# Optimization experiments

Hardware: AMD Instinct MI355X
Metric: run time of the kernel (lower is better)

The kernel has to match this reference:

```python
import jax, jax.numpy as jnp
import numpy as np

B, N, D = 4, 4096, 256

def setup_inputs() -> dict:
    key = jax.random.key(0)
    ks = jax.random.split(key, 7)
    def xavier(k, shape):
        fan_in, fan_out = shape[1], shape[0]
        a = jnp.sqrt(6.0 / (fan_in + fan_out))
        return jax.random.uniform(k, shape, jnp.float32, -a, a)
    return {
        "x": jax.random.normal(ks[0], (B, N, D), jnp.float32),
        "Wq": xavier(ks[1], (D, D)),
        "bq": jnp.zeros((D,), jnp.float32),
        "Wk": xavier(ks[2], (D, D)),
        "bk": jnp.zeros((D,), jnp.float32),
        "Wv": xavier(ks[3], (D, D)),
        "bv": jnp.zeros((D,), jnp.float32),
        "scale": jnp.asarray([jnp.sqrt(jnp.float32(D))]),
    }

def reference(x, Wq, bq, Wk, bk, Wv, bv, scale):
    # nn.Linear: y = x @ W.T + b
    q = jnp.einsum('bnd,ed->bne', x, Wq) + bq
    k = jnp.einsum('bnd,ed->bne', x, Wk) + bk
    v = jnp.einsum('bnd,ed->bne', x, Wv) + bv
    scores = jnp.einsum('bqd,bkd->bqk', q, k) / scale[0]  # [B,N,N]
    attn = jax.nn.softmax(scores, axis=-1)
    out = jnp.einsum('bqk,bkd->bqd', attn, v)
    return out
```

## Files before the change

### kernel.cpp

```cpp
#include <hip/hip_runtime.h>
#include <hip/hip_bf16.h>

typedef unsigned int u32;
typedef unsigned short u16;
typedef __attribute__((ext_vector_type(8))) __bf16 bf8v;
typedef __attribute__((ext_vector_type(16))) float f32x16;
typedef __attribute__((ext_vector_type(8))) u16 u16x8;

__device__ inline u16 f2bf(float f) {
    u32 u = __float_as_uint(f);
    u = (u + 0x7FFF + ((u >> 16) & 1)) >> 16;
    return (u16)u;
}
__device__ inline u32 pk2(float a, float b) {
    return (u32)f2bf(a) | ((u32)f2bf(b) << 16);
}
__device__ inline float bf2f(u16 h) { return __uint_as_float(((u32)h) << 16); }

__device__ inline void dma16(const u16* g, u16* l) {
    __builtin_amdgcn_global_load_lds(
        (const __attribute__((address_space(1))) void*)g,
        (__attribute__((address_space(3))) void*)l, 16, 0, 0);
}

__global__ void cvt_x(const float* __restrict__ src, u16* __restrict__ dst) {
    int g = blockIdx.x * 256 + threadIdx.x;
    int row = g >> 5, cp = g & 31;
    const float* s = src + row * 256 + cp * 8;
    float4 a = *(const float4*)s;
    float4 b = *(const float4*)(s + 4);
    uint4 o;
    o.x = pk2(a.x, a.y); o.y = pk2(a.z, a.w);
    o.z = pk2(b.x, b.y); o.w = pk2(b.z, b.w);
    *(uint4*)(dst + (row >> 5) * 8192 + cp * 256 + (row & 31) * 8) = o;
}

__global__ void cvt_w(const float* __restrict__ wq, const float* __restrict__ wk,
                      const float* __restrict__ wv, u16* __restrict__ dst) {
    const int m = blockIdx.x >> 5;
    const float* src = m == 0 ? wq : m == 1 ? wk : wv;
    int i = ((blockIdx.x & 31) * 256 + threadIdx.x) * 8;
    float4 a = *(const float4*)(src + i);
    float4 b = *(const float4*)(src + i + 4);
    uint4 o;
    o.x = pk2(a.x, a.y); o.y = pk2(a.z, a.w);
    o.z = pk2(b.x, b.y); o.w = pk2(b.z, b.w);
    *(uint4*)(dst + m * 65536 + i) = o;
}

__global__ __launch_bounds__(256) void qkv_proj(
    const u16* __restrict__ xp, const u16* __restrict__ wall,
    const float* __restrict__ bq, const float* __restrict__ bk, const float* __restrict__ bv,
    u16* __restrict__ qp, u16* __restrict__ kp, u16* __restrict__ vp)
{
    const int blk = blockIdx.x;
    const int xcd = blk & 7;
    const int s2 = blk >> 3;
    const int rt = s2 / 12;
    const int yz = s2 % 12;
    const int sel = yz >> 2;
    const int colbase = (yz & 3) * 64;
    const int rowbase0 = (xcd * 16 + rt) * 128;

    const u16* w = wall + sel * 65536;
    const float* bias = sel == 0 ? bq : sel == 1 ? bk : bv;
    const int tid = threadIdx.x;
    const int wave = tid >> 6, lane = tid & 63;
    const int l31 = lane & 31, l5 = lane >> 5;
    const int tg = (rowbase0 >> 5) + wave;

    f32x16 acc0, acc1;
#pragma unroll
    for (int j = 0; j < 16; j++) { acc0[j] = 0.f; acc1[j] = 0.f; }

    const u16* ap  = xp + tg * 8192 + l5 * 256 + l31 * 8;
    const u16* bp0 = w + (colbase + l31) * 256 + l5 * 8;
    const u16* bp1 = bp0 + 32 * 256;
#pragma unroll
    for (int kk = 0; kk < 16; kk++) {
        bf8v af = *(const bf8v*)(ap + kk * 512);
        bf8v b0 = *(const bf8v*)(bp0 + kk * 16);
        bf8v b1 = *(const bf8v*)(bp1 + kk * 16);
        acc0 = __builtin_amdgcn_mfma_f32_32x32x16_bf16(af, b0, acc0, 0, 0, 0);
        acc1 = __builtin_amdgcn_mfma_f32_32x32x16_bf16(af, b1, acc1, 0, 0, 0);
    }

    const float bias0 = bias[colbase + l31], bias1 = bias[colbase + 32 + l31];
    if (sel < 2) {
        u16* base = (sel == 0 ? qp : kp) + tg * 8192;
        const int c0 = (colbase >> 3) + (l31 >> 3), j0 = l31 & 7;
#pragma unroll
        for (int r = 0; r < 16; r++) {
            const int R = (r & 3) + 8 * (r >> 2) + 4 * l5;
            base[c0 * 256 + R * 8 + j0]       = f2bf(acc0[r] + bias0);
            base[(c0 + 4) * 256 + R * 8 + j0] = f2bf(acc1[r] + bias1);
        }
    } else {
        u16* base = vp + tg * 8192;
        const int d0 = colbase + l31, d1 = d0 + 32;
#pragma unroll
        for (int r = 0; r < 16; r++) {
            const int R = (r & 3) + 8 * (r >> 2) + 4 * l5;
            base[(R >> 3) * 2048 + d0 * 8 + (R & 7)] = f2bf(acc0[r] + bias0);
            base[(R >> 3) * 2048 + d1 * 8 + (R & 7)] = f2bf(acc1[r] + bias1);
        }
    }
}

__global__ __launch_bounds__(256, 2) void flash_attn(
    const u16* __restrict__ qp_, const u16* __restrict__ kp_, const u16* __restrict__ vp_,
    const float* __restrict__ scale,
    u16* __restrict__ Opb, float* __restrict__ ml)
{
    __shared__ u16 Ks[2 * 8192];
    __shared__ u16 Vs[2 * 8192];
    __shared__ u16 Ps[4 * 1152];

    const int tid = threadIdx.x;
    const int wave = tid >> 6, lane = tid & 63;
    const int l31 = lane & 31, l5 = lane >> 5;

    const int blk = blockIdx.x;
    const int slot = blk >> 3;
    const int g = (blk & 7) * 2 + (slot >> 5);
    const int qtile = slot & 31;
    const int b = g >> 2, s = g & 3;
    const int qbase = qtile * 128 + wave * 32;
    const float inv_scale = 1.0f / scale[0];

    union { u16x8 u; bf8v v; } oneu;
#pragma unroll
    for (int j = 0; j < 8; j++) oneu.u[j] = 0x3F80;
    const bf8v ones = oneu.v;

    bf8v qf[16];
    {
        const u16* qp = qp_ + (b * 128 + qtile * 4 + wave) * 8192 + l31 * 8;
#pragma unroll
        for (int kk = 0; kk < 16; kk++)
            qf[kk] = *(const bf8v*)(qp + (kk * 2 + l5) * 256);
    }

    f32x16 o[8];
#pragma unroll
    for (int i = 0; i < 8; i++)
#pragma unroll
        for (int j = 0; j < 16; j++) o[i][j] = 0.f;
    f32x16 ls;
#pragma unroll
    for (int j = 0; j < 16; j++) ls[j] = 0.f;

    const u16* kbase = kp_ + (b * 128 + s * 32) * 8192;
    const u16* vbase = vp_ + (b * 128 + s * 32) * 8192;
    u16* pw = Ps + wave * 1152;

#pragma unroll
    for (int j = 0; j < 4; j++) {
        const int i = wave * 4 + j;
        dma16(kbase + i * 512 + lane * 8, Ks + i * 512);
    }
#pragma unroll
    for (int j = 0; j < 4; j++) {
        const int i = wave * 4 + j;
        dma16(vbase + i * 512 + lane * 8, Vs + i * 512);
    }
#pragma unroll
    for (int j = 0; j < 4; j++) {
        const int i = wave * 4 + j;
        dma16(kbase + 8192 + i * 512 + lane * 8, Ks + 8192 + i * 512);
    }
    asm volatile("s_waitcnt vmcnt(8)" ::: "memory");
    asm volatile("s_barrier" ::: "memory");

    bf8v pf0, pf1;
    {
        f32x16 c;
#pragma unroll
        for (int j = 0; j < 16; j++) c[j] = 0.f;
#pragma unroll
        for (int kk = 0; kk < 16; kk++) {
            bf8v kf = *(const bf8v*)(Ks + (kk * 2 + l5) * 256 + l31 * 8);
            c = __builtin_amdgcn_mfma_f32_32x32x16_bf16(qf[kk], kf, c, 0, 0, 0);
        }
#pragma unroll
        for (int r = 0; r < 16; r++) {
            const int R = (r & 3) + 8 * (r >> 2) + 4 * l5;
            pw[R * 36 + l31] = f2bf(__expf(c[r] * inv_scale));
        }
        asm volatile("s_waitcnt lgkmcnt(0)" ::: "memory");
        pf0 = *(const bf8v*)(pw + l31 * 36 + l5 * 8);
        pf1 = *(const bf8v*)(pw + l31 * 36 + 16 + l5 * 8);
    }

#pragma unroll 1
    for (int it = 0; it < 31; it++) {
        const int buf = it & 1;
        asm volatile("s_waitcnt vmcnt(0)" ::: "memory");
        asm volatile("s_barrier" ::: "memory");
        {
            const u16* vt_ = vbase + (it + 1) * 8192;
#pragma unroll
            for (int j = 0; j < 4; j++) {
                const int i = wave * 4 + j;
                dma16(vt_ + i * 512 + lane * 8, Vs + (buf ^ 1) * 8192 + i * 512);
            }
            if (it < 30) {
                const u16* kt_ = kbase + (it + 2) * 8192;
#pragma unroll
                for (int j = 0; j < 4; j++) {
                    const int i = wave * 4 + j;
                    dma16(kt_ + i * 512 + lane * 8, Ks + buf * 8192 + i * 512);
                }
            }
        }
        const u16* Vb_ = Vs + buf * 8192;
        const u16* Kb_ = Ks + (buf ^ 1) * 8192;
        f32x16 c;
#pragma unroll
        for (int j = 0; j < 16; j++) c[j] = 0.f;
        ls = __builtin_amdgcn_mfma_f32_32x32x16_bf16(pf0, ones, ls, 0, 0, 0);
        ls = __builtin_amdgcn_mfma_f32_32x32x16_bf16(pf1, ones, ls, 0, 0, 0);
#pragma unroll
        for (int j = 0; j < 8; j++) {
            bf8v kf0 = *(const bf8v*)(Kb_ + (j * 4 + l5) * 256 + l31 * 8);
            bf8v vf0 = *(const bf8v*)(Vb_ + (l5 * 256 + j * 32 + l31) * 8);
            c = __builtin_amdgcn_mfma_f32_32x32x16_bf16(qf[2 * j], kf0, c, 0, 0, 0);
            o[j] = __builtin_amdgcn_mfma_f32_32x32x16_bf16(pf0, vf0, o[j], 0, 0, 0);
            bf8v kf1 = *(const bf8v*)(Kb_ + (j * 4 + 2 + l5) * 256 + l31 * 8);
            bf8v vf1 = *(const bf8v*)(Vb_ + ((2 + l5) * 256 + j * 32 + l31) * 8);
            c = __builtin_amdgcn_mfma_f32_32x32x16_bf16(qf[2 * j + 1], kf1, c, 0, 0, 0);
            o[j] = __builtin_amdgcn_mfma_f32_32x32x16_bf16(pf1, vf1, o[j], 0, 0, 0);
        }
#pragma unroll
        for (int r = 0; r < 16; r++) {
            const int R = (r & 3) + 8 * (r >> 2) + 4 * l5;
            pw[R * 36 + l31] = f2bf(__expf(c[r] * inv_scale));
        }
        asm volatile("s_waitcnt lgkmcnt(0)" ::: "memory");
        pf0 = *(const bf8v*)(pw + l31 * 36 + l5 * 8);
        pf1 = *(const bf8v*)(pw + l31 * 36 + 16 + l5 * 8);
    }

    asm volatile("s_waitcnt vmcnt(0)" ::: "memory");
    asm volatile("s_barrier" ::: "memory");
    {
        const u16* Vb_ = Vs + 8192;
        ls = __builtin_amdgcn_mfma_f32_32x32x16_bf16(pf0, ones, ls, 0, 0, 0);
        ls = __builtin_amdgcn_mfma_f32_32x32x16_bf16(pf1, ones, ls, 0, 0, 0);
#pragma unroll
        for (int j = 0; j < 8; j++) {
            bf8v vf0 = *(const bf8v*)(Vb_ + (l5 * 256 + j * 32 + l31) * 8);
            o[j] = __builtin_amdgcn_mfma_f32_32x32x16_bf16(pf0, vf0, o[j], 0, 0, 0);
            bf8v vf1 = *(const bf8v*)(Vb_ + ((2 + l5) * 256 + j * 32 + l31) * 8);
            o[j] = __builtin_amdgcn_mfma_f32_32x32x16_bf16(pf1, vf1, o[j], 0, 0, 0);
        }
    }

    const int rowg = s * 16384 + b * 4096 + qbase;
    u16* ob = Opb + (size_t)rowg * 256;
#pragma unroll
    for (int nb = 0; nb < 8; nb++)
#pragma unroll
        for (int r = 0; r < 16; r++) {
            const int R = (r & 3) + 8 * (r >> 2) + 4 * l5;
            ob[R * 256 + nb * 32 + l31] = f2bf(o[nb][r]);
        }
    if (l31 == 0)
#pragma unroll
        for (int r = 0; r < 16; r++) {
            const int R = (r & 3) + 8 * (r >> 2) + 4 * l5;
            ml[rowg + R] = ls[r];
        }
}

__global__ __launch_bounds__(256) void combine(
    const u16* __restrict__ Opb, const float* __restrict__ ml, float* __restrict__ out)
{
    const int row = blockIdx.x * 4 + (threadIdx.x >> 6);
    const int lane = threadIdx.x & 63;
    const float denom = ml[row] + ml[16384 + row] + ml[32768 + row] + ml[49152 + row];
    float4 acc = {0.f, 0.f, 0.f, 0.f};
#pragma unroll
    for (int si = 0; si < 4; si++) {
        ushort4 v = *(const ushort4*)(Opb + ((size_t)si * 16384 + row) * 256 + lane * 4);
        acc.x += bf2f(v.x); acc.y += bf2f(v.y);
        acc.z += bf2f(v.z); acc.w += bf2f(v.w);
    }
    const float inv = 1.0f / denom;
    acc.x *= inv; acc.y *= inv; acc.z *= inv; acc.w *= inv;
    *((float4*)(out + (size_t)row * 256) + lane) = acc;
}

extern "C" void kernel_launch(void* const* d_in, const int* in_sizes, int n_in,
                              void* d_out, int out_size, void* d_ws, size_t ws_size,
                              hipStream_t stream) {
    const float* x     = (const float*)d_in[0];
    const float* Wq    = (const float*)d_in[1];
    const float* bq    = (const float*)d_in[2];
    const float* Wk    = (const float*)d_in[3];
    const float* bk    = (const float*)d_in[4];
    const float* Wv    = (const float*)d_in[5];
    const float* bv    = (const float*)d_in[6];
    const float* scale = (const float*)d_in[7];
    float* out = (float*)d_out;

    char* ws = (char*)d_ws;
    u16* xp   = (u16*)ws;
    u16* qp   = (u16*)(ws + (8u  << 20));
    u16* kp   = (u16*)(ws + (16u << 20));
    u16* vp   = (u16*)(ws + (24u << 20));
    u16* wall = (u16*)(ws + (32u << 20));
    u16* Opb  = (u16*)(ws + (34u << 20));
    float* ml = (float*)(ws + (66u << 20));

    cvt_x<<<2048, 256, 0, stream>>>(x, xp);
    cvt_w<<<96, 256, 0, stream>>>(Wq, Wk, Wv, wall);
    qkv_proj<<<1536, 256, 0, stream>>>(xp, wall, bq, bk, bv, qp, kp, vp);
    flash_attn<<<512, 256, 0, stream>>>(qp, kp, vp, scale, Opb, ml);
    combine<<<4096, 256, 0, stream>>>(Opb, ml, out);
}
```

Baseline: 201.5 us.

## Merge conversion kernels, stage swizzled weights in LDS, reorder QK/PV in flash loop

Merges the x and weight conversion kernels into one launch, and writes the converted weights in an XOR-swizzled layout. The projection kernel then DMAs its 64-column weight slice into shared memory and reads the B fragments from LDS instead of global memory. The flash attention loop now runs the full QK^T MFMA chain first, then interleaves the exp/bf16 P writes with the PV MFMAs. Together these aim to cut launch overhead and global weight traffic and to give the scheduler more overlap, at the cost of an extra barrier and 32KB LDS per projection block.

```diff
diff --git a/kernel.cpp b/kernel.cpp
--- a/kernel.cpp
+++ b/kernel.cpp
@@ -23,29 +23,35 @@
         (__attribute__((address_space(3))) void*)l, 16, 0, 0);
 }
 
-__global__ void cvt_x(const float* __restrict__ src, u16* __restrict__ dst) {
-    int g = blockIdx.x * 256 + threadIdx.x;
-    int row = g >> 5, cp = g & 31;
-    const float* s = src + row * 256 + cp * 8;
-    float4 a = *(const float4*)s;
-    float4 b = *(const float4*)(s + 4);
-    uint4 o;
-    o.x = pk2(a.x, a.y); o.y = pk2(a.z, a.w);
-    o.z = pk2(b.x, b.y); o.w = pk2(b.z, b.w);
-    *(uint4*)(dst + (row >> 5) * 8192 + cp * 256 + (row & 31) * 8) = o;
-}
-
-__global__ void cvt_w(const float* __restrict__ wq, const float* __restrict__ wk,
-                      const float* __restrict__ wv, u16* __restrict__ dst) {
-    const int m = blockIdx.x >> 5;
-    const float* src = m == 0 ? wq : m == 1 ? wk : wv;
-    int i = ((blockIdx.x & 31) * 256 + threadIdx.x) * 8;
-    float4 a = *(const float4*)(src + i);
-    float4 b = *(const float4*)(src + i + 4);
-    uint4 o;
-    o.x = pk2(a.x, a.y); o.y = pk2(a.z, a.w);
-    o.z = pk2(b.x, b.y); o.w = pk2(b.z, b.w);
-    *(uint4*)(dst + m * 65536 + i) = o;
+__global__ void cvt_all(const float* __restrict__ x,
+                        const float* __restrict__ wq, const float* __restrict__ wk,
+                        const float* __restrict__ wv,
+                        u16* __restrict__ xp, u16* __restrict__ wall) {
+    const int blk = blockIdx.x;
+    if (blk < 2048) {
+        int g = blk * 256 + threadIdx.x;
+        int row = g >> 5, cp = g & 31;
+        const float* s = x + row * 256 + cp * 8;
+        float4 a = *(const float4*)s;
+        float4 b = *(const float4*)(s + 4);
+        uint4 o;
+        o.x = pk2(a.x, a.y); o.y = pk2(a.z, a.w);
+        o.z = pk2(b.x, b.y); o.w = pk2(b.z, b.w);
+        *(uint4*)(xp + (row >> 5) * 8192 + cp * 256 + (row & 31) * 8) = o;
+    } else {
+        const int bb = blk - 2048;
+        const int m = bb >> 5;
+        const float* src = m == 0 ? wq : m == 1 ? wk : wv;
+        int g = (bb & 31) * 256 + threadIdx.x;
+        int row = g >> 5, c = g & 31;
+        const float* s = src + row * 256 + c * 8;
+        float4 a = *(const float4*)s;
+        float4 b = *(const float4*)(s + 4);
+        uint4 o;
+        o.x = pk2(a.x, a.y); o.y = pk2(a.z, a.w);
+        o.z = pk2(b.x, b.y); o.w = pk2(b.z, b.w);
+        *(uint4*)(wall + m * 65536 + row * 256 + ((c ^ (row & 7)) * 8)) = o;
+    }
 }
 
 __global__ __launch_bounds__(256) void qkv_proj(
@@ -53,6 +59,8 @@
     const float* __restrict__ bq, const float* __restrict__ bk, const float* __restrict__ bv,
     u16* __restrict__ qp, u16* __restrict__ kp, u16* __restrict__ vp)
 {
+    __shared__ u16 Ws[64 * 256];
+
     const int blk = blockIdx.x;
     const int xcd = blk & 7;
     const int s2 = blk >> 3;
@@ -62,25 +70,34 @@
     const int colbase = (yz & 3) * 64;
     const int rowbase0 = (xcd * 16 + rt) * 128;
 
-    const u16* w = wall + sel * 65536;
     const float* bias = sel == 0 ? bq : sel == 1 ? bk : bv;
     const int tid = threadIdx.x;
     const int wave = tid >> 6, lane = tid & 63;
     const int l31 = lane & 31, l5 = lane >> 5;
     const int tg = (rowbase0 >> 5) + wave;
 
+    {
+        const u16* wsrc = wall + sel * 65536 + colbase * 256;
+#pragma unroll
+        for (int j = 0; j < 8; j++) {
+            const int i = wave * 8 + j;
+            dma16(wsrc + i * 512 + lane * 8, Ws + i * 512);
+        }
+    }
+    asm volatile("s_waitcnt vmcnt(0)" ::: "memory");
+    __syncthreads();
+
     f32x16 acc0, acc1;
 #pragma unroll
     for (int j = 0; j < 16; j++) { acc0[j] = 0.f; acc1[j] = 0.f; }
 
-    const u16* ap  = xp + tg * 8192 + l5 * 256 + l31 * 8;
-    const u16* bp0 = w + (colbase + l31) * 256 + l5 * 8;
-    const u16* bp1 = bp0 + 32 * 256;
+    const u16* ap = xp + tg * 8192 + l5 * 256 + l31 * 8;
+    const int sw = l31 & 7;
 #pragma unroll
     for (int kk = 0; kk < 16; kk++) {
         bf8v af = *(const bf8v*)(ap + kk * 512);
-        bf8v b0 = *(const bf8v*)(bp0 + kk * 16);
-        bf8v b1 = *(const bf8v*)(bp1 + kk * 16);
+        bf8v b0 = *(const bf8v*)(Ws + l31 * 256 + (((kk * 2 + l5) ^ sw) * 8));
+        bf8v b1 = *(const bf8v*)(Ws + (32 + l31) * 256 + (((kk * 2 + l5) ^ sw) * 8));
         acc0 = __builtin_amdgcn_mfma_f32_32x32x16_bf16(af, b0, acc0, 0, 0, 0);
         acc1 = __builtin_amdgcn_mfma_f32_32x32x16_bf16(af, b1, acc1, 0, 0, 0);
     }
@@ -213,28 +230,34 @@
                 }
             }
         }
-        const u16* Vb_ = Vs + buf * 8192;
         const u16* Kb_ = Ks + (buf ^ 1) * 8192;
         f32x16 c;
 #pragma unroll
         for (int j = 0; j < 16; j++) c[j] = 0.f;
+#pragma unroll
+        for (int kk = 0; kk < 16; kk++) {
+            bf8v kf = *(const bf8v*)(Kb_ + (kk * 2 + l5) * 256 + l31 * 8);
+            c = __builtin_amdgcn_mfma_f32_32x32x16_bf16(qf[kk], kf, c, 0, 0, 0);
+        }
+        const u16* Vb_ = Vs + buf * 8192;
         ls = __builtin_amdgcn_mfma_f32_32x32x16_bf16(pf0, ones, ls, 0, 0, 0);
         ls = __builtin_amdgcn_mfma_f32_32x32x16_bf16(pf1, ones, ls, 0, 0, 0);
 #pragma unroll
         for (int j = 0; j < 8; j++) {
-            bf8v kf0 = *(const bf8v*)(Kb_ + (j * 4 + l5) * 256 + l31 * 8);
             bf8v vf0 = *(const bf8v*)(Vb_ + (l5 * 256 + j * 32 + l31) * 8);
-            c = __builtin_amdgcn_mfma_f32_32x32x16_bf16(qf[2 * j], kf0, c, 0, 0, 0);
             o[j] = __builtin_amdgcn_mfma_f32_32x32x16_bf16(pf0, vf0, o[j], 0, 0, 0);
-            bf8v kf1 = *(const bf8v*)(Kb_ + (j * 4 + 2 + l5) * 256 + l31 * 8);
+            {
+                const int r = 2 * j;
+                const int R = (r & 3) + 8 * (r >> 2) + 4 * l5;
+                pw[R * 36 + l31] = f2bf(__expf(c[r] * inv_scale));
+            }
             bf8v vf1 = *(const bf8v*)(Vb_ + ((2 + l5) * 256 + j * 32 + l31) * 8);
-            c = __builtin_amdgcn_mfma_f32_32x32x16_bf16(qf[2 * j + 1], kf1, c, 0, 0, 0);
             o[j] = __builtin_amdgcn_mfma_f32_32x32x16_bf16(pf1, vf1, o[j], 0, 0, 0);
-        }
-#pragma unroll
-        for (int r = 0; r < 16; r++) {
-            const int R = (r & 3) + 8 * (r >> 2) + 4 * l5;
-            pw[R * 36 + l31] = f2bf(__expf(c[r] * inv_scale));
+            {
+                const int r = 2 * j + 1;
+                const int R = (r & 3) + 8 * (r >> 2) + 4 * l5;
+                pw[R * 36 + l31] = f2bf(__expf(c[r] * inv_scale));
+            }
         }
         asm volatile("s_waitcnt lgkmcnt(0)" ::: "memory");
         pf0 = *(const bf8v*)(pw + l31 * 36 + l5 * 8);
@@ -313,8 +336,7 @@
     u16* Opb  = (u16*)(ws + (34u << 20));
     float* ml = (float*)(ws + (66u << 20));
 
-    cvt_x<<<2048, 256, 0, stream>>>(x, xp);
-    cvt_w<<<96, 256, 0, stream>>>(Wq, Wk, Wv, wall);
+    cvt_all<<<2144, 256, 0, stream>>>(x, Wq, Wk, Wv, xp, wall);
     qkv_proj<<<1536, 256, 0, stream>>>(xp, wall, bq, bk, bv, qp, kp, vp);
     flash_attn<<<512, 256, 0, stream>>>(qp, kp, vp, scale, Opb, ml);
     combine<<<4096, 256, 0, stream>>>(Opb, ml, out);
```

After: 187.1 us. 7.1% less time.
